# Kernel optimization log

Measured on AMD Instinct MI355X. Metric: run time of the kernel, lower is better.

## Reference

```python
import jax, jax.numpy as jnp
import numpy as np

NUM_CLASSES = 512  # P distinct identities in the batch (labels are in [0, P))
TAU = 0.5
EPS = 1e-12


def _l2norm(x):
    # F.normalize(x, dim=1) with eps clamp
    n = jnp.sqrt(jnp.sum(x * x, axis=1, keepdims=True))
    return x / jnp.maximum(n, EPS)


def setup_inputs() -> dict:
    key = jax.random.key(0)
    k1, k2, k3 = jax.random.split(key, 3)
    N, D, P = 8192, 2048, NUM_CLASSES
    feat_vp = jax.random.normal(k1, (N, D), dtype=jnp.float32)
    feat_ap = jax.random.normal(k2, (N, D), dtype=jnp.float32)
    feat_rp = jax.random.normal(k3, (N, D), dtype=jnp.float32)
    # P identities, K = N/P instances each; every class present
    label = (jnp.arange(N) % P).astype(jnp.int32)
    return {"feat_vp": feat_vp, "feat_ap": feat_ap, "feat_rp": feat_rp, "label": label}


def reference(feat_vp, feat_ap, feat_rp, label):
    P = NUM_CLASSES
    fv = _l2norm(feat_vp)
    fa = _l2norm(feat_ap)
    fr = _l2norm(feat_rp)

    # segment-mean over labels (replaces the O(N^2 D) python loop)
    counts = jax.ops.segment_sum(jnp.ones_like(label, dtype=fv.dtype), label,
                                 num_segments=P)  # [P]
    inv_cnt = 1.0 / counts[:, None]

    def centers(f):
        s = jax.ops.segment_sum(f, label, num_segments=P)  # [P, D]
        return _l2norm(s * inv_cnt)

    cv, ca, cr = centers(fv), centers(fa), centers(fr)

    # per-sample centers = unique centers gathered back by label
    loss_intra = (jnp.sum((fv - cv[label]) ** 2, axis=1).mean()
                  + jnp.sum((fa - ca[label]) ** 2, axis=1).mean()
                  + jnp.sum((fr - cr[label]) ** 2, axis=1).mean())

    def pair_loss(c1, c2):
        logits = (c1 @ c2.T) / TAU  # [P, P]
        logp = jax.nn.log_softmax(logits, axis=1)
        return -jnp.mean(jnp.diagonal(logp))

    loss_inter = pair_loss(cv, ca) + pair_loss(cv, cr) + pair_loss(ca, cr)
    return loss_intra + loss_inter
```

## Files before the change

kernel.cpp:

```cpp
#include <hip/hip_runtime.h>
#include <hip/hip_bf16.h>

#define P_CLS 512
#define D_DIM 2048
#define CAP   32
#define TAU_INV 2.0f

typedef short short8 __attribute__((ext_vector_type(8)));
typedef float f32x4 __attribute__((ext_vector_type(4)));

__device__ __forceinline__ unsigned short f2bf_bits(float x) {
  __hip_bfloat16 b = __float2bfloat16(x);
  unsigned short u;
  __builtin_memcpy(&u, &b, sizeof(u));
  return u;
}

__device__ __forceinline__ float xred_sum(float v) {
#pragma unroll
  for (int o = 1; o < 64; o <<= 1) v += __shfl_xor(v, o, 64);
  return v;
}
__device__ __forceinline__ float xred_max(float v) {
#pragma unroll
  for (int o = 1; o < 64; o <<= 1) v = fmaxf(v, __shfl_xor(v, o, 64));
  return v;
}

__global__ __launch_bounds__(1024)
void k_prep(const int* __restrict__ label, int* __restrict__ cnt,
            int* __restrict__ idx, float* __restrict__ accs, int n) {
  __shared__ int lcnt[P_CLS];
  int t = threadIdx.x;
  if (t < P_CLS) lcnt[t] = 0;
  if (t >= P_CLS && t < P_CLS + 8) accs[t - P_CLS] = 0.f;
  __syncthreads();
  for (int i = t; i < n; i += 1024) {
    int p = label[i];
    int slot = atomicAdd(&lcnt[p], 1);
    if (slot < CAP) idx[p * CAP + slot] = i;
  }
  __syncthreads();
  if (t < P_CLS) cnt[t] = lcnt[t];
}

__global__ __launch_bounds__(256)
void k_centers(const float* __restrict__ f0, const float* __restrict__ f1,
               const float* __restrict__ f2, const int* __restrict__ cnt,
               const int* __restrict__ idx, __hip_bfloat16* __restrict__ cb,
               float* __restrict__ accs) {
  __shared__ float scr[2][4];
  __shared__ float s2s[4];
  int p = blockIdx.x, m = blockIdx.y;
  const float* F = (m == 0) ? f0 : (m == 1) ? f1 : f2;
  int t = threadIdx.x, lane = t & 63, wv = t >> 6;
  int c = cnt[p];
  if (c > CAP) c = CAP;
  const int* idxp = idx + p * CAP;
  int col0 = wv * 512 + lane * 4;
  f32x4 acc0 = {0, 0, 0, 0}, acc1 = {0, 0, 0, 0};
  if (c > 0) {
    const float* rp0 = F + (long)idxp[0] * D_DIM;
    f32x4 v0 = *(const f32x4*)(rp0 + col0);
    f32x4 v1 = *(const f32x4*)(rp0 + col0 + 256);
    f32x4 n10 = {0,0,0,0}, n11 = {0,0,0,0};
    if (c > 1) {
      const float* rp1 = F + (long)idxp[1] * D_DIM;
      n10 = *(const f32x4*)(rp1 + col0);
      n11 = *(const f32x4*)(rp1 + col0 + 256);
    }
    for (int r = 0; r < c; ++r) {
      f32x4 n20 = {0,0,0,0}, n21 = {0,0,0,0};
      if (r + 2 < c) {
        const float* rp2 = F + (long)idxp[r + 2] * D_DIM;
        n20 = *(const f32x4*)(rp2 + col0);
        n21 = *(const f32x4*)(rp2 + col0 + 256);
      }
      f32x4 q = v0 * v0 + v1 * v1;
      float ssq = q.x + q.y + q.z + q.w;
      ssq = xred_sum(ssq);
      if (lane == 0) scr[r & 1][wv] = ssq;
      __syncthreads();
      float tot = scr[r & 1][0] + scr[r & 1][1] + scr[r & 1][2] + scr[r & 1][3];
      float w = 1.0f / fmaxf(sqrtf(tot), 1e-12f);
      acc0 += v0 * w;
      acc1 += v1 * w;
      v0 = n10; v1 = n11;
      n10 = n20; n11 = n21;
    }
  }
  f32x4 q = acc0 * acc0 + acc1 * acc1;
  float s2 = q.x + q.y + q.z + q.w;
  s2 = xred_sum(s2);
  if (lane == 0) s2s[wv] = s2;
  __syncthreads();
  float sn = sqrtf(s2s[0] + s2s[1] + s2s[2] + s2s[3]);
  float inv = 1.0f / fmaxf(sn, 1e-12f);
  __hip_bfloat16* dst = cb + ((long)m * P_CLS + p) * D_DIM;
  f32x4 o0 = acc0 * inv, o1 = acc1 * inv;
  ushort4 h0, h1;
  h0.x = f2bf_bits(o0.x); h0.y = f2bf_bits(o0.y);
  h0.z = f2bf_bits(o0.z); h0.w = f2bf_bits(o0.w);
  h1.x = f2bf_bits(o1.x); h1.y = f2bf_bits(o1.y);
  h1.z = f2bf_bits(o1.z); h1.w = f2bf_bits(o1.w);
  *(ushort4*)(dst + col0) = h0;
  *(ushort4*)(dst + col0 + 256) = h1;
  if (t == 0 && c > 0) atomicAdd(&accs[0], sn);
}

__global__ __launch_bounds__(256)
void k_gemm(const __hip_bfloat16* __restrict__ cbh, float* __restrict__ logits) {
  __shared__ __align__(16) unsigned short As[2][64 * 40], Bs[2][64 * 40];
  int pair = blockIdx.y, kz = blockIdx.z, nkz = gridDim.z;
  int ksl = D_DIM / nkz;
  int ma = (pair == 2) ? 1 : 0;
  int mb = (pair == 0) ? 1 : 2;
  const unsigned short* A =
      (const unsigned short*)cbh + (long)ma * P_CLS * D_DIM + kz * ksl;
  const unsigned short* B =
      (const unsigned short*)cbh + (long)mb * P_CLS * D_DIM + kz * ksl;
  float* C = logits + ((long)kz * 3 + pair) * P_CLS * P_CLS;
  int tm = (blockIdx.x >> 3) * 64, tn = (blockIdx.x & 7) * 64;
  int t = threadIdx.x, lane = t & 63, wv = t >> 6;
  int srow = t >> 2, skc = (t & 3) * 8;
  int quad = lane >> 4, mr = lane & 15;
  const unsigned short* pa = A + (long)(tm + srow) * D_DIM + skc;
  const unsigned short* pb = B + (long)(tn + srow) * D_DIM + skc;
  f32x4 acc[4] = {{0,0,0,0},{0,0,0,0},{0,0,0,0},{0,0,0,0}};
  uint4 av = *(const uint4*)pa, bv = *(const uint4*)pb;
  *(uint4*)(&As[0][srow * 40 + skc]) = av;
  *(uint4*)(&Bs[0][srow * 40 + skc]) = bv;
  av = *(const uint4*)(pa + 32); bv = *(const uint4*)(pb + 32);
  const int NIT = ksl / 32;
  for (int it = 0; it < NIT; ++it) {
    __syncthreads();
    int cur = it & 1;
    if (it + 1 < NIT) {
      *(uint4*)(&As[cur ^ 1][srow * 40 + skc]) = av;
      *(uint4*)(&Bs[cur ^ 1][srow * 40 + skc]) = bv;
    }
    if (it + 2 < NIT) {
      av = *(const uint4*)(pa + (it + 2) * 32);
      bv = *(const uint4*)(pb + (it + 2) * 32);
    }
    short8 af = *(const short8*)(&As[cur][(wv * 16 + mr) * 40 + quad * 8]);
#pragma unroll
    for (int nb = 0; nb < 4; ++nb) {
      short8 bfr = *(const short8*)(&Bs[cur][(nb * 16 + mr) * 40 + quad * 8]);
      acc[nb] = __builtin_amdgcn_mfma_f32_16x16x32_bf16(af, bfr, acc[nb], 0, 0, 0);
    }
  }
  int crow = tm + wv * 16 + quad * 4;
#pragma unroll
  for (int nb = 0; nb < 4; ++nb)
#pragma unroll
    for (int r = 0; r < 4; ++r)
      C[(long)(crow + r) * P_CLS + tn + nb * 16 + mr] = acc[nb][r] * TAU_INV;
}

__global__ __launch_bounds__(256)
void k_lse(const float* __restrict__ logits, float* __restrict__ accs, int nkz,
           float* __restrict__ out, float invN) {
  __shared__ float sred[8];
  int row = blockIdx.x;
  int p = row & (P_CLS - 1);
  int t = threadIdx.x, lane = t & 63, wv = t >> 6;
  float v0 = 0.f, v1 = 0.f;
  for (int z = 0; z < nkz; ++z) {
    const float* L = logits + ((long)z * 3 * P_CLS + row) * P_CLS;
    v0 += L[t];
    v1 += L[t + 256];
  }
  float mx = xred_max(fmaxf(v0, v1));
  if (lane == 0) sred[wv] = mx;
  __syncthreads();
  mx = fmaxf(fmaxf(sred[0], sred[1]), fmaxf(sred[2], sred[3]));
  float e = expf(v0 - mx) + expf(v1 - mx);
  e = xred_sum(e);
  if (lane == 0) sred[4 + wv] = e;
  __syncthreads();
  if (t == 0) {
    float tot = sred[4] + sred[5] + sred[6] + sred[7];
    float diag = 0.f;
    for (int z = 0; z < nkz; ++z)
      diag += logits[((long)z * 3 * P_CLS + row) * P_CLS + p];
    atomicAdd(&accs[1], mx + logf(tot) - diag);
    __threadfence();
    int old = atomicAdd((int*)&accs[2], 1);
    if (old == gridDim.x - 1) {
      float li = atomicAdd(&accs[1], 0.f);
      float ls = atomicAdd(&accs[0], 0.f);
      out[0] = 6.0f - 2.0f * invN * ls + li * (1.0f / (float)P_CLS);
    }
  }
}

extern "C" void kernel_launch(void* const* d_in, const int* in_sizes, int n_in,
                              void* d_out, int out_size, void* d_ws, size_t ws_size,
                              hipStream_t stream) {
  const float* fvp = (const float*)d_in[0];
  const float* fap = (const float*)d_in[1];
  const float* frp = (const float*)d_in[2];
  const int* label = (const int*)d_in[3];
  int N = in_sizes[3];

  char* ws = (char*)d_ws;
  int* cnt = (int*)ws;
  int* idx = (int*)(ws + 2048);
  float* accs = (float*)(ws + 2048 + 65536);
  __hip_bfloat16* cb = (__hip_bfloat16*)(ws + 131072);
  float* logits = (float*)(ws + 131072 + 3ul * P_CLS * D_DIM * 2);

  size_t base = 131072 + 3ul * P_CLS * D_DIM * 2;
  size_t per_z = 3ul * P_CLS * P_CLS * 4;
  int KZ = (ws_size >= base + 4 * per_z) ? 4 : 2;

  hipLaunchKernelGGL(k_prep, dim3(1), dim3(1024), 0, stream, label, cnt, idx,
                     accs, N);
  hipLaunchKernelGGL(k_centers, dim3(P_CLS, 3), dim3(256), 0, stream,
                     fvp, fap, frp, cnt, idx, cb, accs);
  hipLaunchKernelGGL(k_gemm, dim3(64, 3, KZ), dim3(256), 0, stream, cb, logits);
  hipLaunchKernelGGL(k_lse, dim3(3 * P_CLS), dim3(256), 0, stream, logits, accs,
                     KZ, (float*)d_out, 1.0f / (float)N);
}
```

Before: 269.3 us.

## Batch 8 rows per group in center accumulation and move final combine to separate kernel

The center kernel now loads 8 sample rows at once, computes their squared norms with interleaved cross-lane reductions, and needs one block barrier per group instead of one per row. This raises memory-level parallelism and cuts synchronisation in the bandwidth-bound phase. It adds a launch-bounds occupancy hint and more register pressure. The last-block atomic counter in the LSE kernel is replaced by a tiny final kernel, which costs one extra launch but removes a fence and an atomic from every block.

After: 249.8 us. 7.2% less time.

```diff
diff --git a/kernel.cpp b/kernel.cpp
--- a/kernel.cpp
+++ b/kernel.cpp
@@ -44,12 +44,12 @@
   if (t < P_CLS) cnt[t] = lcnt[t];
 }
 
-__global__ __launch_bounds__(256)
+__global__ __launch_bounds__(256, 4)
 void k_centers(const float* __restrict__ f0, const float* __restrict__ f1,
                const float* __restrict__ f2, const int* __restrict__ cnt,
                const int* __restrict__ idx, __hip_bfloat16* __restrict__ cb,
                float* __restrict__ accs) {
-  __shared__ float scr[2][4];
+  __shared__ f32x4 scr[2][4][2];
   __shared__ float s2s[4];
   int p = blockIdx.x, m = blockIdx.y;
   const float* F = (m == 0) ? f0 : (m == 1) ? f1 : f2;
@@ -59,34 +59,48 @@
   const int* idxp = idx + p * CAP;
   int col0 = wv * 512 + lane * 4;
   f32x4 acc0 = {0, 0, 0, 0}, acc1 = {0, 0, 0, 0};
-  if (c > 0) {
-    const float* rp0 = F + (long)idxp[0] * D_DIM;
-    f32x4 v0 = *(const f32x4*)(rp0 + col0);
-    f32x4 v1 = *(const f32x4*)(rp0 + col0 + 256);
-    f32x4 n10 = {0,0,0,0}, n11 = {0,0,0,0};
-    if (c > 1) {
-      const float* rp1 = F + (long)idxp[1] * D_DIM;
-      n10 = *(const f32x4*)(rp1 + col0);
-      n11 = *(const f32x4*)(rp1 + col0 + 256);
-    }
-    for (int r = 0; r < c; ++r) {
-      f32x4 n20 = {0,0,0,0}, n21 = {0,0,0,0};
-      if (r + 2 < c) {
-        const float* rp2 = F + (long)idxp[r + 2] * D_DIM;
-        n20 = *(const f32x4*)(rp2 + col0);
-        n21 = *(const f32x4*)(rp2 + col0 + 256);
+  int ng = (c + 7) >> 3;
+  for (int g = 0; g < ng; ++g) {
+    int rbase = g * 8;
+    f32x4 v0[8], v1[8];
+#pragma unroll
+    for (int j = 0; j < 8; ++j) {
+      int rr = rbase + j;
+      if (rr >= c) rr = c - 1;
+      const float* rp = F + (long)idxp[rr] * D_DIM + col0;
+      v0[j] = *(const f32x4*)rp;
+      v1[j] = *(const f32x4*)(rp + 256);
+    }
+    f32x4 sa, sb;
+#pragma unroll
+    for (int j = 0; j < 4; ++j) {
+      f32x4 qa = v0[j] * v0[j] + v1[j] * v1[j];
+      sa[j] = qa.x + qa.y + qa.z + qa.w;
+      f32x4 qb = v0[j + 4] * v0[j + 4] + v1[j + 4] * v1[j + 4];
+      sb[j] = qb.x + qb.y + qb.z + qb.w;
+    }
+#pragma unroll
+    for (int o = 1; o < 64; o <<= 1) {
+#pragma unroll
+      for (int j = 0; j < 4; ++j) {
+        sa[j] += __shfl_xor(sa[j], o, 64);
+        sb[j] += __shfl_xor(sb[j], o, 64);
       }
-      f32x4 q = v0 * v0 + v1 * v1;
-      float ssq = q.x + q.y + q.z + q.w;
-      ssq = xred_sum(ssq);
-      if (lane == 0) scr[r & 1][wv] = ssq;
-      __syncthreads();
-      float tot = scr[r & 1][0] + scr[r & 1][1] + scr[r & 1][2] + scr[r & 1][3];
-      float w = 1.0f / fmaxf(sqrtf(tot), 1e-12f);
-      acc0 += v0 * w;
-      acc1 += v1 * w;
-      v0 = n10; v1 = n11;
-      n10 = n20; n11 = n21;
+    }
+    int par = g & 1;
+    if (lane == 0) {
+      scr[par][wv][0] = sa;
+      scr[par][wv][1] = sb;
+    }
+    __syncthreads();
+    f32x4 ta = scr[par][0][0] + scr[par][1][0] + scr[par][2][0] + scr[par][3][0];
+    f32x4 tb = scr[par][0][1] + scr[par][1][1] + scr[par][2][1] + scr[par][3][1];
+#pragma unroll
+    for (int j = 0; j < 8; ++j) {
+      float tot = (j < 4) ? ta[j] : tb[j - 4];
+      float w = (rbase + j < c) ? (1.0f / fmaxf(sqrtf(tot), 1e-12f)) : 0.f;
+      acc0 += v0[j] * w;
+      acc1 += v1[j] * w;
     }
   }
   f32x4 q = acc0 * acc0 + acc1 * acc1;
@@ -159,8 +173,7 @@
 }
 
 __global__ __launch_bounds__(256)
-void k_lse(const float* __restrict__ logits, float* __restrict__ accs, int nkz,
-           float* __restrict__ out, float invN) {
+void k_lse(const float* __restrict__ logits, float* __restrict__ accs, int nkz) {
   __shared__ float sred[8];
   int row = blockIdx.x;
   int p = row & (P_CLS - 1);
@@ -185,14 +198,12 @@
     for (int z = 0; z < nkz; ++z)
       diag += logits[((long)z * 3 * P_CLS + row) * P_CLS + p];
     atomicAdd(&accs[1], mx + logf(tot) - diag);
-    __threadfence();
-    int old = atomicAdd((int*)&accs[2], 1);
-    if (old == gridDim.x - 1) {
-      float li = atomicAdd(&accs[1], 0.f);
-      float ls = atomicAdd(&accs[0], 0.f);
-      out[0] = 6.0f - 2.0f * invN * ls + li * (1.0f / (float)P_CLS);
-    }
-  }
+  }
+}
+
+__global__ void k_final(const float* __restrict__ accs, float* __restrict__ out,
+                        float invN) {
+  out[0] = 6.0f - 2.0f * invN * accs[0] + accs[1] * (1.0f / (float)P_CLS);
 }
 
 extern "C" void kernel_launch(void* const* d_in, const int* in_sizes, int n_in,
@@ -220,6 +231,7 @@
   hipLaunchKernelGGL(k_centers, dim3(P_CLS, 3), dim3(256), 0, stream,
                      fvp, fap, frp, cnt, idx, cb, accs);
   hipLaunchKernelGGL(k_gemm, dim3(64, 3, KZ), dim3(256), 0, stream, cb, logits);
-  hipLaunchKernelGGL(k_lse, dim3(3 * P_CLS), dim3(256), 0, stream, logits, accs,
-                     KZ, (float*)d_out, 1.0f / (float)N);
-}
+  hipLaunchKernelGGL(k_lse, dim3(3 * P_CLS), dim3(256), 0, stream, logits, accs, KZ);
+  hipLaunchKernelGGL(k_final, dim3(1), dim3(1), 0, stream, accs, (float*)d_out,
+                     1.0f / (float)N);
+}
```
